# Optimization experiments

Hardware: AMD Instinct MI355X
Metric: run time of the kernel (lower is better)

Reference implementation:

```python
import jax, jax.numpy as jnp
import numpy as np

NUM_GRAPHS = 32   # point clouds per batch
PTS = 1024        # points per cloud (equal-size graphs; batch = node_idx // PTS)
NUM_FEAT = 14
DIM = 64
K = 30            # kNN includes the self-edge (distance 0), as torch_cluster.knn does


def _edge_conv(xb, W1, b1, W2, b2):
    # xb: [B, P, F] node features, per-graph dynamic kNN EdgeConv with max aggregation
    s = jnp.sum(xb * xb, axis=-1)                                   # [B, P]
    d = s[:, :, None] + s[:, None, :] - 2.0 * jnp.einsum('bpf,bqf->bpq', xb, xb)
    idx = jax.lax.top_k(-d, K)[1]                                   # [B, P, K]
    xj = jax.vmap(lambda xg, ig: xg[ig])(xb, idx)                   # [B, P, K, F]
    xi = xb[:, :, None, :]
    e = jnp.concatenate([jnp.broadcast_to(xi, xj.shape), xj - xi], axis=-1)  # [B,P,K,2F]
    h = jax.nn.relu(e @ W1 + b1)
    h = jax.nn.relu(h @ W2 + b2)
    return jnp.max(h, axis=2)                                       # [B, P, DIM]


def setup_inputs() -> dict:
    key = jax.random.key(0)
    ks = jax.random.split(key, 24)
    N = NUM_GRAPHS * PTS

    def w(i, shape):
        scale = shape[0] ** -0.5 if len(shape) > 1 else 0.02
        return jax.random.normal(ks[i], shape, jnp.float32) * scale

    return dict(
        x=jax.random.normal(ks[0], (N, NUM_FEAT), jnp.float32),
        batch=jnp.arange(N, dtype=jnp.int32) // PTS,
        c1w1=w(1, (2 * NUM_FEAT, DIM)), c1b1=w(2, (DIM,)), c1w2=w(3, (DIM, DIM)), c1b2=w(4, (DIM,)),
        c2w1=w(5, (2 * DIM, DIM)), c2b1=w(6, (DIM,)), c2w2=w(7, (DIM, DIM)), c2b2=w(8, (DIM,)),
        c3w1=w(9, (2 * DIM, DIM)), c3b1=w(10, (DIM,)), c3w2=w(11, (DIM, DIM)), c3b2=w(12, (DIM,)),
        lw=w(13, (3 * DIM, 1024)), lb=w(14, (1024,)),
        hw1=w(15, (1024, 256)), hb1=w(16, (256,)),
        hw2=w(17, (256, 128)), hb2=w(18, (128,)),
        hw3=w(19, (128, DIM)), hb3=w(20, (DIM,)),
    )


def reference(x, batch, c1w1, c1b1, c1w2, c1b2, c2w1, c2b1, c2w2, c2b2,
              c3w1, c3b1, c3w2, c3b2, lw, lb, hw1, hb1, hw2, hb2, hw3, hb3):
    # batch encodes equal-size graphs of PTS nodes -> reshape to [B, P, F]
    xb = x.reshape(NUM_GRAPHS, PTS, -1)
    x1 = _edge_conv(xb, c1w1, c1b1, c1w2, c1b2)
    x2 = _edge_conv(x1, c2w1, c2b1, c2w2, c2b2)
    x3 = _edge_conv(x2, c3w1, c3b1, c3w2, c3b2)
    h = jnp.concatenate([x1, x2, x3], axis=-1).reshape(-1, 3 * DIM)  # [N, 192]
    h = jax.nn.relu(h @ lw + lb)      # lin1: MLP([3*dim, 1024])
    h = jax.nn.relu(h @ hw1 + hb1)    # MLP([1024, 256]); dropout = identity at eval
    h = jax.nn.relu(h @ hw2 + hb2)    # MLP([256, 128]); dropout = identity at eval
    return h @ hw3 + hb3              # Lin(128, dim)
```

## Files before the change

kernel.cpp:

```cpp
#include <hip/hip_runtime.h>
#include <hip/hip_bf16.h>
#include <float.h>

#define NG    32
#define PTS   1024
#define NPTS  (NG*PTS)
#define KNN   30
#define DIM   64
#define CHUNK 8192

typedef __attribute__((ext_vector_type(8))) short bf16x8;
typedef __attribute__((ext_vector_type(4))) float f32x4;
typedef unsigned short ushort_t;

template<int F>
__global__ __launch_bounds__(256) void prep_k(const float* __restrict__ X, int ldx,
                                              float* __restrict__ S32,
                                              double* __restrict__ S64,
                                              float* __restrict__ XT) {
    int p = blockIdx.x * 256 + threadIdx.x;
    float s32 = 0.f;
    double s64 = 0.0;
    #pragma unroll
    for (int f = 0; f < F; ++f) {
        float v = X[(size_t)p * ldx + f];
        s32 = fmaf(v, v, s32);
        s64 = fma((double)v, (double)v, s64);
        XT[(size_t)f * NPTS + p] = v;
    }
    S32[p] = s32;
    S64[p] = s64;
}

__global__ __launch_bounds__(256) void smax_k(const float* __restrict__ S32,
                                              float* __restrict__ SMAX,
                                              int* __restrict__ ovf_cnt) {
    if (blockIdx.x == 0 && threadIdx.x == 0) *ovf_cnt = 0;
    int g = blockIdx.x;
    int lane = threadIdx.x & 63, wv = threadIdx.x >> 6;
    float m = 0.f;
    for (int t = threadIdx.x; t < PTS; t += 256) m = fmaxf(m, S32[(size_t)g * PTS + t]);
    #pragma unroll
    for (int off = 32; off; off >>= 1) m = fmaxf(m, __shfl_xor(m, off));
    __shared__ float wm[4];
    if (lane == 0) wm[wv] = m;
    __syncthreads();
    if (threadIdx.x == 0)
        SMAX[g] = fmaxf(fmaxf(wm[0], wm[1]), fmaxf(wm[2], wm[3]));
}

template<int F>
__global__ __launch_bounds__(256) void knn_k(const float* __restrict__ X, int ldx,
                                             const float* __restrict__ XT,
                                             const float* __restrict__ S32,
                                             const double* __restrict__ S64,
                                             const float* __restrict__ SMAX,
                                             int* __restrict__ IDX,
                                             int* __restrict__ ovf_cnt,
                                             int* __restrict__ ovf_list) {
    constexpr int FP = (F + 3) & ~3;
    int wv = threadIdx.x >> 6;
    int lane = threadIdx.x & 63;
    int i0 = blockIdx.x * 16;
    int base = i0 & ~(PTS - 1);
    __shared__ __align__(16) float xis[16][FP];
    __shared__ int surv[4][4][64];
    for (int l = threadIdx.x; l < 16 * F; l += 256) {
        int pt = l / F, f = l - pt * F;
        xis[pt][f] = X[(size_t)(i0 + pt) * ldx + f];
    }
    __syncthreads();

    float si[4];
    #pragma unroll
    for (int ii = 0; ii < 4; ++ii) si[ii] = S32[i0 + wv * 4 + ii];
    float smax = SMAX[i0 >> 10];

    float d32[4][16];
    #pragma unroll
    for (int ii = 0; ii < 4; ++ii)
        #pragma unroll
        for (int r = 0; r < 16; ++r) d32[ii][r] = 0.f;

    constexpr int F4 = F & ~3;
    for (int f4 = 0; f4 < F4; f4 += 4) {
        float4 xi[4];
        #pragma unroll
        for (int ii = 0; ii < 4; ++ii)
            xi[ii] = *reinterpret_cast<const float4*>(&xis[wv * 4 + ii][f4]);
        #pragma unroll
        for (int fo = 0; fo < 4; ++fo) {
            int f = f4 + fo;
            #pragma unroll
            for (int m = 0; m < 4; ++m) {
                const float4 xj = *reinterpret_cast<const float4*>(
                    &XT[(size_t)f * NPTS + base + (m << 8) + (lane << 2)]);
                #pragma unroll
                for (int ii = 0; ii < 4; ++ii) {
                    float xif = (fo == 0) ? xi[ii].x : (fo == 1) ? xi[ii].y
                               : (fo == 2) ? xi[ii].z : xi[ii].w;
                    d32[ii][m * 4 + 0] = fmaf(xif, xj.x, d32[ii][m * 4 + 0]);
                    d32[ii][m * 4 + 1] = fmaf(xif, xj.y, d32[ii][m * 4 + 1]);
                    d32[ii][m * 4 + 2] = fmaf(xif, xj.z, d32[ii][m * 4 + 2]);
                    d32[ii][m * 4 + 3] = fmaf(xif, xj.w, d32[ii][m * 4 + 3]);
                }
            }
        }
    }
    for (int f = F4; f < F; ++f) {
        float xif[4];
        #pragma unroll
        for (int ii = 0; ii < 4; ++ii) xif[ii] = xis[wv * 4 + ii][f];
        #pragma unroll
        for (int m = 0; m < 4; ++m) {
            const float4 xj = *reinterpret_cast<const float4*>(
                &XT[(size_t)f * NPTS + base + (m << 8) + (lane << 2)]);
            #pragma unroll
            for (int ii = 0; ii < 4; ++ii) {
                d32[ii][m * 4 + 0] = fmaf(xif[ii], xj.x, d32[ii][m * 4 + 0]);
                d32[ii][m * 4 + 1] = fmaf(xif[ii], xj.y, d32[ii][m * 4 + 1]);
                d32[ii][m * 4 + 2] = fmaf(xif[ii], xj.z, d32[ii][m * 4 + 2]);
                d32[ii][m * 4 + 3] = fmaf(xif[ii], xj.w, d32[ii][m * 4 + 3]);
            }
        }
    }
    #pragma unroll
    for (int m = 0; m < 4; ++m) {
        const float4 sj = *reinterpret_cast<const float4*>(&S32[base + (m << 8) + (lane << 2)]);
        #pragma unroll
        for (int ii = 0; ii < 4; ++ii) {
            d32[ii][m * 4 + 0] = (si[ii] + sj.x) - 2.f * d32[ii][m * 4 + 0];
            d32[ii][m * 4 + 1] = (si[ii] + sj.y) - 2.f * d32[ii][m * 4 + 1];
            d32[ii][m * 4 + 2] = (si[ii] + sj.z) - 2.f * d32[ii][m * 4 + 2];
            d32[ii][m * 4 + 3] = (si[ii] + sj.w) - 2.f * d32[ii][m * 4 + 3];
        }
    }

    const unsigned long long below = (1ull << lane) - 1;
    #pragma unroll
    for (int ii = 0; ii < 4; ++ii) {
        int i = i0 + wv * 4 + ii;
        float lo = -1.f, hi = 2.f * (si[ii] + smax) + 1.f;
        for (int it = 0; it < 32; ++it) {
            float piv = 0.5f * (lo + hi);
            int cnt = 0;
            #pragma unroll
            for (int r = 0; r < 16; ++r)
                cnt += __popcll(__ballot(d32[ii][r] <= piv));
            if (cnt >= KNN) { hi = piv; if (cnt <= 56) break; }
            else lo = piv;
        }
        float T = hi + 1.6e-5f * (si[ii] + smax);

        int total = 0;
        #pragma unroll
        for (int r = 0; r < 16; ++r) {
            bool pred = d32[ii][r] <= T;
            unsigned long long mask = __ballot(pred);
            if (pred) {
                int slot = total + __popcll(mask & below);
                if (slot < 64)
                    surv[wv][ii][slot] = ((r >> 2) << 8) + (lane << 2) + (r & 3);
            }
            total += __popcll(mask);
        }
        if (total > 64) {
            if (lane == 0) ovf_list[atomicAdd(ovf_cnt, 1)] = i;
            continue;
        }
        __builtin_amdgcn_wave_barrier();
        asm volatile("s_waitcnt lgkmcnt(0)" ::: "memory");

        double d64 = DBL_MAX;
        int jabs = 0x7fffffff;
        if (lane < total) {
            int jl = surv[wv][ii][lane];
            jabs = base + jl;
            const float* xj = X + (size_t)jabs * ldx;
            double dot = 0.0;
            #pragma unroll
            for (int f = 0; f < F; ++f)
                dot = fma((double)xis[wv * 4 + ii][f], (double)xj[f], dot);
            d64 = (S64[i] + S64[jabs]) - 2.0 * dot;
        }
        #pragma unroll
        for (int k = 2; k <= 64; k <<= 1) {
            #pragma unroll
            for (int s = k >> 1; s > 0; s >>= 1) {
                double od = __shfl_xor(d64, s);
                int oj = __shfl_xor(jabs, s);
                bool otherSmaller = (od < d64) || (od == d64 && oj < jabs);
                bool keepSmaller = (((lane & k) == 0) == ((lane & s) == 0));
                if (otherSmaller == keepSmaller) { d64 = od; jabs = oj; }
            }
        }
        if (lane < KNN) IDX[(size_t)i * KNN + lane] = jabs;
        __builtin_amdgcn_wave_barrier();
    }
}

template<int F>
__global__ __launch_bounds__(256) void fb_k(const float* __restrict__ X, int ldx,
                                            const float* __restrict__ XT,
                                            const double* __restrict__ S64,
                                            int* __restrict__ IDX,
                                            const int* __restrict__ ovf_cnt,
                                            const int* __restrict__ ovf_list) {
    int wv = threadIdx.x >> 6, lane = threadIdx.x & 63;
    int novf = *ovf_cnt;
    __shared__ double xis[4][F];
    for (int t = blockIdx.x * 4 + wv; t < novf; t += 64 * 4) {
        int i = ovf_list[t];
        int base = i & ~(PTS - 1);
        if (lane < F) xis[wv][lane] = (double)X[(size_t)i * ldx + lane];
        __builtin_amdgcn_wave_barrier();
        asm volatile("s_waitcnt lgkmcnt(0)" ::: "memory");
        double dd[16];
        #pragma unroll
        for (int m = 0; m < 4; ++m) {
            int j0 = (m << 8) + (lane << 2);
            double d0 = 0.0, d1 = 0.0, d2 = 0.0, d3 = 0.0;
            #pragma unroll
            for (int f = 0; f < F; ++f) {
                double xif = xis[wv][f];
                const float4 xj = *reinterpret_cast<const float4*>(&XT[(size_t)f * NPTS + base + j0]);
                d0 = fma(xif, (double)xj.x, d0);
                d1 = fma(xif, (double)xj.y, d1);
                d2 = fma(xif, (double)xj.z, d2);
                d3 = fma(xif, (double)xj.w, d3);
            }
            dd[m * 4 + 0] = (S64[i] + S64[base + j0 + 0]) - 2.0 * d0;
            dd[m * 4 + 1] = (S64[i] + S64[base + j0 + 1]) - 2.0 * d1;
            dd[m * 4 + 2] = (S64[i] + S64[base + j0 + 2]) - 2.0 * d2;
            dd[m * 4 + 3] = (S64[i] + S64[base + j0 + 3]) - 2.0 * d3;
        }
        for (int k = 0; k < KNN; ++k) {
            double bd = DBL_MAX;
            int bj = 0x7fffffff;
            #pragma unroll
            for (int r = 0; r < 16; ++r) {
                int j = ((r >> 2) << 8) + (lane << 2) + (r & 3);
                if (dd[r] < bd) { bd = dd[r]; bj = j; }
            }
            #pragma unroll
            for (int off = 32; off; off >>= 1) {
                double od = __shfl_xor(bd, off);
                int oj = __shfl_xor(bj, off);
                if (od < bd || (od == bd && oj < bj)) { bd = od; bj = oj; }
            }
            if (((bj >> 2) & 63) == lane) {
                int r = ((bj >> 8) << 2) | (bj & 3);
                #pragma unroll
                for (int rr = 0; rr < 16; ++rr) if (rr == r) dd[rr] = DBL_MAX;
            }
            if (lane == 0) IDX[(size_t)i * KNN + k] = base + bj;
        }
        __builtin_amdgcn_wave_barrier();
    }
}

template<int F>
__global__ __launch_bounds__(256) void mg_k(const float* __restrict__ X, int ldx,
                                            const float* __restrict__ W1,
                                            const float* __restrict__ B1,
                                            float* __restrict__ Mo, float* __restrict__ Go) {
    int tid = blockIdx.x * 256 + threadIdx.x;
    int pp = tid >> 6, c = tid & 63;
    float m = B1[c], g = 0.f;
    #pragma unroll
    for (int f = 0; f < F; ++f) {
        float xv = X[(size_t)pp * ldx + f];
        float wt = W1[f * DIM + c];
        float wb = W1[(F + f) * DIM + c];
        m = fmaf(xv, wt - wb, m);
        g = fmaf(xv, wb, g);
    }
    Mo[(size_t)pp * DIM + c] = m;
    Go[(size_t)pp * DIM + c] = g;
}

__global__ __launch_bounds__(256) void edge_k(const int* __restrict__ IDX,
                                              const float* __restrict__ G,
                                              const float* __restrict__ Mb,
                                              const float* __restrict__ W2,
                                              const float* __restrict__ B2,
                                              float* __restrict__ OUT, int ldo) {
    __shared__ ushort_t w2hi[64][72], w2lo[64][72];
    __shared__ ushort_t h1hi[4][32][72], h1lo[4][32][72];
    int wv = threadIdx.x >> 6, lane = threadIdx.x & 63;
    int i = blockIdx.x * 4 + wv;
    int col16 = lane & 15, grp = lane >> 4, grp8 = (lane >> 4) << 3;

    for (int l = threadIdx.x; l < 4096; l += 256) {
        int c = l & 63, k = l >> 6;
        float w = W2[k * 64 + c];
        __hip_bfloat16 bh = __float2bfloat16(w);
        __hip_bfloat16 bl = __float2bfloat16(w - __bfloat162float(bh));
        w2hi[c][k] = *reinterpret_cast<ushort_t*>(&bh);
        w2lo[c][k] = *reinterpret_cast<ushort_t*>(&bl);
    }
    __syncthreads();

    float mi = Mb[(size_t)i * DIM + lane];
    const int* idxrow = IDX + (size_t)i * KNN;
    int idxv = (lane < KNN) ? idxrow[lane] : 0;
    float g[KNN];
    #pragma unroll
    for (int nb = 0; nb < KNN; ++nb) {
        int j = __shfl(idxv, nb);
        g[nb] = G[(size_t)j * DIM + lane];
    }
    #pragma unroll
    for (int nb = 0; nb < KNN; ++nb) {
        float h = fmaxf(mi + g[nb], 0.f);
        __hip_bfloat16 bh = __float2bfloat16(h);
        __hip_bfloat16 bl = __float2bfloat16(h - __bfloat162float(bh));
        h1hi[wv][nb][lane] = *reinterpret_cast<ushort_t*>(&bh);
        h1lo[wv][nb][lane] = *reinterpret_cast<ushort_t*>(&bl);
    }
    h1hi[wv][30][lane] = 0; h1lo[wv][30][lane] = 0;
    h1hi[wv][31][lane] = 0; h1lo[wv][31][lane] = 0;
    __builtin_amdgcn_wave_barrier();
    asm volatile("s_waitcnt lgkmcnt(0)" ::: "memory");

    bf16x8 ahi[2][2], alo[2][2];
    #pragma unroll
    for (int m = 0; m < 2; ++m)
        #pragma unroll
        for (int ks = 0; ks < 2; ++ks) {
            ahi[m][ks] = *reinterpret_cast<const bf16x8*>(&h1hi[wv][m * 16 + col16][ks * 32 + grp8]);
            alo[m][ks] = *reinterpret_cast<const bf16x8*>(&h1lo[wv][m * 16 + col16][ks * 32 + grp8]);
        }

    float myout = 0.f;
    #pragma unroll
    for (int n = 0; n < 4; ++n) {
        bf16x8 bhi[2], blo[2];
        #pragma unroll
        for (int ks = 0; ks < 2; ++ks) {
            bhi[ks] = *reinterpret_cast<const bf16x8*>(&w2hi[n * 16 + col16][ks * 32 + grp8]);
            blo[ks] = *reinterpret_cast<const bf16x8*>(&w2lo[n * 16 + col16][ks * 32 + grp8]);
        }
        f32x4 acc0 = {0.f, 0.f, 0.f, 0.f}, acc1 = {0.f, 0.f, 0.f, 0.f};
        #pragma unroll
        for (int ks = 0; ks < 2; ++ks) {
            acc0 = __builtin_amdgcn_mfma_f32_16x16x32_bf16(ahi[0][ks], bhi[ks], acc0, 0, 0, 0);
            acc1 = __builtin_amdgcn_mfma_f32_16x16x32_bf16(ahi[1][ks], bhi[ks], acc1, 0, 0, 0);
            acc0 = __builtin_amdgcn_mfma_f32_16x16x32_bf16(ahi[0][ks], blo[ks], acc0, 0, 0, 0);
            acc1 = __builtin_amdgcn_mfma_f32_16x16x32_bf16(ahi[1][ks], blo[ks], acc1, 0, 0, 0);
            acc0 = __builtin_amdgcn_mfma_f32_16x16x32_bf16(alo[0][ks], bhi[ks], acc0, 0, 0, 0);
            acc1 = __builtin_amdgcn_mfma_f32_16x16x32_bf16(alo[1][ks], bhi[ks], acc1, 0, 0, 0);
        }
        float cm = fmaxf(fmaxf(acc0[0], acc0[1]), fmaxf(acc0[2], acc0[3]));
        cm = fmaxf(cm, fmaxf(acc1[0], acc1[1]));
        if (grp < 3) cm = fmaxf(cm, fmaxf(acc1[2], acc1[3]));
        cm = fmaxf(cm, __shfl_xor(cm, 16));
        cm = fmaxf(cm, __shfl_xor(cm, 32));
        if (grp == n) myout = cm;
    }
    OUT[(size_t)i * ldo + lane] = fmaxf(myout + B2[lane], 0.f);
}

template<int TM, int TN, int BK, bool RELU>
__global__ __launch_bounds__(256) void gemm_k(const float* __restrict__ A, int Kd,
                                              const float* __restrict__ W, int N,
                                              const float* __restrict__ Bias,
                                              float* __restrict__ C) {
    constexpr int MM = TM / 16, MN = TN / 16;
    __shared__ __align__(16) float As_t[BK][TM + 4];
    __shared__ __align__(16) float Ws[BK][TN];
    int bm = blockIdx.y * TM, bn = blockIdx.x * TN;
    int tid = threadIdx.x;
    int tr = tid >> 4, tc = tid & 15;
    float acc[MM][MN] = {};
    for (int k0 = 0; k0 < Kd; k0 += BK) {
        #pragma unroll
        for (int l = tid; l < TM * (BK / 4); l += 256) {
            int r = l / (BK / 4), q = l & (BK / 4 - 1);
            const float4 a4 = *reinterpret_cast<const float4*>(&A[(size_t)(bm + r) * Kd + k0 + 4 * q]);
            As_t[4 * q + 0][r] = a4.x;
            As_t[4 * q + 1][r] = a4.y;
            As_t[4 * q + 2][r] = a4.z;
            As_t[4 * q + 3][r] = a4.w;
        }
        #pragma unroll
        for (int l = tid; l < BK * (TN / 4); l += 256) {
            int r = l / (TN / 4), q = l & (TN / 4 - 1);
            *reinterpret_cast<float4*>(&Ws[r][4 * q]) =
                *reinterpret_cast<const float4*>(&W[(size_t)(k0 + r) * N + bn + 4 * q]);
        }
        __syncthreads();
        #pragma unroll
        for (int kk = 0; kk < BK; ++kk) {
            float a[MM], w[MN];
            #pragma unroll
            for (int u = 0; u < MM; u += 4) {
                const float4 v4 = *reinterpret_cast<const float4*>(&As_t[kk][tr * MM + u]);
                a[u] = v4.x; a[u + 1] = v4.y; a[u + 2] = v4.z; a[u + 3] = v4.w;
            }
            #pragma unroll
            for (int v = 0; v < MN; v += 4) {
                const float4 v4 = *reinterpret_cast<const float4*>(&Ws[kk][tc * MN + v]);
                w[v] = v4.x; w[v + 1] = v4.y; w[v + 2] = v4.z; w[v + 3] = v4.w;
            }
            #pragma unroll
            for (int u = 0; u < MM; ++u)
                #pragma unroll
                for (int v = 0; v < MN; ++v)
                    acc[u][v] = fmaf(a[u], w[v], acc[u][v]);
        }
        __syncthreads();
    }
    #pragma unroll
    for (int u = 0; u < MM; ++u) {
        int row = bm + tr * MM + u;
        #pragma unroll
        for (int v = 0; v < MN; v += 4) {
            int col = bn + tc * MN + v;
            float4 o;
            o.x = acc[u][v + 0] + Bias[col + 0];
            o.y = acc[u][v + 1] + Bias[col + 1];
            o.z = acc[u][v + 2] + Bias[col + 2];
            o.w = acc[u][v + 3] + Bias[col + 3];
            if (RELU) {
                o.x = fmaxf(o.x, 0.f); o.y = fmaxf(o.y, 0.f);
                o.z = fmaxf(o.z, 0.f); o.w = fmaxf(o.w, 0.f);
            }
            *reinterpret_cast<float4*>(&C[(size_t)row * N + col]) = o;
        }
    }
}

template<int F>
static void run_conv(const float* Xin, int ldx,
                     const float* W1, const float* B1,
                     const float* W2, const float* B2,
                     float* OUT, int ldo,
                     float* XT, float* S32, double* S64, float* SMAX,
                     float* Mb, float* Gb, int* IDX,
                     int* ovf_cnt, int* ovf_list,
                     hipStream_t stream) {
    prep_k<F><<<NPTS / 256, 256, 0, stream>>>(Xin, ldx, S32, S64, XT);
    smax_k<<<NG, 256, 0, stream>>>(S32, SMAX, ovf_cnt);
    knn_k<F><<<NPTS / 16, 256, 0, stream>>>(Xin, ldx, XT, S32, S64, SMAX, IDX,
                                            ovf_cnt, ovf_list);
    fb_k<F><<<64, 256, 0, stream>>>(Xin, ldx, XT, S64, IDX, ovf_cnt, ovf_list);
    mg_k<F><<<NPTS * DIM / 256, 256, 0, stream>>>(Xin, ldx, W1, B1, Mb, Gb);
    edge_k<<<NPTS / 4, 256, 0, stream>>>(IDX, Gb, Mb, W2, B2, OUT, ldo);
}

extern "C" void kernel_launch(void* const* d_in, const int* in_sizes, int n_in,
                              void* d_out, int out_size, void* d_ws, size_t ws_size,
                              hipStream_t stream) {
    (void)in_sizes; (void)n_in; (void)out_size; (void)ws_size;
    const float* x    = (const float*)d_in[0];
    const float* c1w1 = (const float*)d_in[2];  const float* c1b1 = (const float*)d_in[3];
    const float* c1w2 = (const float*)d_in[4];  const float* c1b2 = (const float*)d_in[5];
    const float* c2w1 = (const float*)d_in[6];  const float* c2b1 = (const float*)d_in[7];
    const float* c2w2 = (const float*)d_in[8];  const float* c2b2 = (const float*)d_in[9];
    const float* c3w1 = (const float*)d_in[10]; const float* c3b1 = (const float*)d_in[11];
    const float* c3w2 = (const float*)d_in[12]; const float* c3b2 = (const float*)d_in[13];
    const float* lw   = (const float*)d_in[14]; const float* lb   = (const float*)d_in[15];
    const float* hw1  = (const float*)d_in[16]; const float* hb1  = (const float*)d_in[17];
    const float* hw2  = (const float*)d_in[18]; const float* hb2  = (const float*)d_in[19];
    const float* hw3  = (const float*)d_in[20]; const float* hb3  = (const float*)d_in[21];
    float* out = (float*)d_out;

    float* XC  = (float*)d_ws;
    int*   IDX = (int*)(XC + (size_t)NPTS * 192);
    int*   ovf_cnt  = IDX + (size_t)NPTS * KNN;
    int*   ovf_list = ovf_cnt + 1;
    float* SCR = (float*)(ovf_list + NPTS + 1);
    float*  XT   = SCR;
    double* S64  = (double*)(XT + (size_t)64 * NPTS);
    float*  S32  = (float*)(S64 + NPTS);
    float*  SMAX = S32 + NPTS;
    float*  Mb   = SMAX + 64;
    float*  Gb   = Mb + (size_t)NPTS * DIM;
    float* H1 = SCR;
    float* H2 = H1 + (size_t)CHUNK * 1024;
    float* H3 = H2 + (size_t)CHUNK * 256;

    run_conv<14>(x,        14,  c1w1, c1b1, c1w2, c1b2, XC + 0,   192,
                 XT, S32, S64, SMAX, Mb, Gb, IDX, ovf_cnt, ovf_list, stream);
    run_conv<64>(XC + 0,   192, c2w1, c2b1, c2w2, c2b2, XC + 64,  192,
                 XT, S32, S64, SMAX, Mb, Gb, IDX, ovf_cnt, ovf_list, stream);
    run_conv<64>(XC + 64,  192, c3w1, c3b1, c3w2, c3b2, XC + 128, 192,
                 XT, S32, S64, SMAX, Mb, Gb, IDX, ovf_cnt, ovf_list, stream);

    for (int ch = 0; ch < 4; ++ch) {
        const float* a0 = XC + (size_t)ch * CHUNK * 192;
        float* o0 = out + (size_t)ch * CHUNK * 64;
        gemm_k<128, 128, 16, true ><<<dim3(1024 / 128, CHUNK / 128), 256, 0, stream>>>(a0, 192,  lw,  1024, lb,  H1);
        gemm_k< 64, 128, 16, true ><<<dim3(256  / 128, CHUNK / 64 ), 256, 0, stream>>>(H1, 1024, hw1, 256,  hb1, H2);
        gemm_k< 64, 128, 16, true ><<<dim3(128  / 128, CHUNK / 64 ), 256, 0, stream>>>(H2, 256,  hw2, 128,  hb2, H3);
        gemm_k< 64,  64, 16, false><<<dim3(64   / 64 , CHUNK / 64 ), 256, 0, stream>>>(H3, 128,  hw3, 64,   hb3, o0);
    }
}
```

Before: 1.616 ms.

## Move the two large head GEMMs to split-bf16 MFMA kernels

Replaces the fp32 SIMT GEMMs for lin1 (192->1024) and the first head layer (1024->256) with a new MFMA kernel that uses a three-term hi/lo bf16 split to stay close to fp32 accuracy. Weights are pre-split and transposed by a small conversion kernel. The 1024-wide intermediate is stored as bf16 hi/lo pairs instead of fp32, which keeps its memory traffic the same while removing reconversion. In exchange it costs extra conversion launches and a small loss of precision from dropping the lo*lo term.

Measured after the change: 1.397 ms. -13.6%, faster.

```diff
diff --git a/kernel.cpp b/kernel.cpp
--- a/kernel.cpp
+++ b/kernel.cpp
@@ -12,6 +12,14 @@
 typedef __attribute__((ext_vector_type(8))) short bf16x8;
 typedef __attribute__((ext_vector_type(4))) float f32x4;
 typedef unsigned short ushort_t;
+
+__device__ inline void bfsplit(float v, ushort_t& h, ushort_t& l) {
+    __hip_bfloat16 bh = __float2bfloat16(v);
+    float r = v - __bfloat162float(bh);
+    __hip_bfloat16 bl = __float2bfloat16(r);
+    h = *reinterpret_cast<ushort_t*>(&bh);
+    l = *reinterpret_cast<ushort_t*>(&bl);
+}
 
 template<int F>
 __global__ __launch_bounds__(256) void prep_k(const float* __restrict__ X, int ldx,
@@ -293,11 +301,7 @@
 
     for (int l = threadIdx.x; l < 4096; l += 256) {
         int c = l & 63, k = l >> 6;
-        float w = W2[k * 64 + c];
-        __hip_bfloat16 bh = __float2bfloat16(w);
-        __hip_bfloat16 bl = __float2bfloat16(w - __bfloat162float(bh));
-        w2hi[c][k] = *reinterpret_cast<ushort_t*>(&bh);
-        w2lo[c][k] = *reinterpret_cast<ushort_t*>(&bl);
+        bfsplit(W2[k * 64 + c], w2hi[c][k], w2lo[c][k]);
     }
     __syncthreads();
 
@@ -313,10 +317,7 @@
     #pragma unroll
     for (int nb = 0; nb < KNN; ++nb) {
         float h = fmaxf(mi + g[nb], 0.f);
-        __hip_bfloat16 bh = __float2bfloat16(h);
-        __hip_bfloat16 bl = __float2bfloat16(h - __bfloat162float(bh));
-        h1hi[wv][nb][lane] = *reinterpret_cast<ushort_t*>(&bh);
-        h1lo[wv][nb][lane] = *reinterpret_cast<ushort_t*>(&bl);
+        bfsplit(h, h1hi[wv][nb][lane], h1lo[wv][nb][lane]);
     }
     h1hi[wv][30][lane] = 0; h1lo[wv][30][lane] = 0;
     h1hi[wv][31][lane] = 0; h1lo[wv][31][lane] = 0;
@@ -359,6 +360,112 @@
         if (grp == n) myout = cm;
     }
     OUT[(size_t)i * ldo + lane] = fmaxf(myout + B2[lane], 0.f);
+}
+
+__global__ __launch_bounds__(256) void wcvt_k(const float* __restrict__ W, int K, int N,
+                                              ushort_t* __restrict__ Th,
+                                              ushort_t* __restrict__ Tl) {
+    int idx = blockIdx.x * 256 + threadIdx.x;
+    if (idx >= K * N) return;
+    int k = idx / N, n = idx - k * N;
+    ushort_t h, l;
+    bfsplit(W[idx], h, l);
+    Th[(size_t)n * K + k] = h;
+    Tl[(size_t)n * K + k] = l;
+}
+
+template<bool A32, bool OUT16, bool RELU>
+__global__ __launch_bounds__(256) void gemmx_k(
+    const float* __restrict__ Afp,
+    const ushort_t* __restrict__ Agh, const ushort_t* __restrict__ Agl, int Kd,
+    const ushort_t* __restrict__ Bth, const ushort_t* __restrict__ Btl,
+    int N, const float* __restrict__ Bias,
+    float* __restrict__ Cfp, ushort_t* __restrict__ Cgh, ushort_t* __restrict__ Cgl) {
+    constexpr int BM = 128, BN = 128, BKP = 40;
+    __shared__ ushort_t Ah[BM][BKP], Al[BM][BKP], Bh[BN][BKP], Bl[BN][BKP];
+    int tid = threadIdx.x;
+    int lane = tid & 63, wv = tid >> 6;
+    int wr = wv >> 1, wc = wv & 1;
+    int col16 = lane & 15, grp = lane >> 4, grp8 = grp << 3;
+    int bm = blockIdx.y * BM, bn = blockIdx.x * BN;
+    f32x4 acc[4][4];
+    #pragma unroll
+    for (int mf = 0; mf < 4; ++mf)
+        #pragma unroll
+        for (int nf = 0; nf < 4; ++nf) acc[mf][nf] = (f32x4){0.f, 0.f, 0.f, 0.f};
+
+    for (int k0 = 0; k0 < Kd; k0 += 32) {
+        if constexpr (A32) {
+            for (int l = tid; l < BM * 8; l += 256) {
+                int r = l >> 3, c4 = (l & 7) << 2;
+                const float4 a = *reinterpret_cast<const float4*>(&Afp[(size_t)(bm + r) * Kd + k0 + c4]);
+                ushort4 h4, l4;
+                bfsplit(a.x, h4.x, l4.x);
+                bfsplit(a.y, h4.y, l4.y);
+                bfsplit(a.z, h4.z, l4.z);
+                bfsplit(a.w, h4.w, l4.w);
+                *reinterpret_cast<ushort4*>(&Ah[r][c4]) = h4;
+                *reinterpret_cast<ushort4*>(&Al[r][c4]) = l4;
+            }
+        } else {
+            for (int l = tid; l < BM * 4; l += 256) {
+                int r = l >> 2, q = (l & 3) << 3;
+                *reinterpret_cast<uint4*>(&Ah[r][q]) =
+                    *reinterpret_cast<const uint4*>(&Agh[(size_t)(bm + r) * Kd + k0 + q]);
+                *reinterpret_cast<uint4*>(&Al[r][q]) =
+                    *reinterpret_cast<const uint4*>(&Agl[(size_t)(bm + r) * Kd + k0 + q]);
+            }
+        }
+        for (int l = tid; l < BN * 4; l += 256) {
+            int n = l >> 2, q = (l & 3) << 3;
+            *reinterpret_cast<uint4*>(&Bh[n][q]) =
+                *reinterpret_cast<const uint4*>(&Bth[(size_t)(bn + n) * Kd + k0 + q]);
+            *reinterpret_cast<uint4*>(&Bl[n][q]) =
+                *reinterpret_cast<const uint4*>(&Btl[(size_t)(bn + n) * Kd + k0 + q]);
+        }
+        __syncthreads();
+
+        bf16x8 afh[4], afl[4], bfh[4], bfl[4];
+        #pragma unroll
+        for (int mf = 0; mf < 4; ++mf) {
+            afh[mf] = *reinterpret_cast<const bf16x8*>(&Ah[wr * 64 + mf * 16 + col16][grp8]);
+            afl[mf] = *reinterpret_cast<const bf16x8*>(&Al[wr * 64 + mf * 16 + col16][grp8]);
+        }
+        #pragma unroll
+        for (int nf = 0; nf < 4; ++nf) {
+            bfh[nf] = *reinterpret_cast<const bf16x8*>(&Bh[wc * 64 + nf * 16 + col16][grp8]);
+            bfl[nf] = *reinterpret_cast<const bf16x8*>(&Bl[wc * 64 + nf * 16 + col16][grp8]);
+        }
+        #pragma unroll
+        for (int mf = 0; mf < 4; ++mf)
+            #pragma unroll
+            for (int nf = 0; nf < 4; ++nf) {
+                acc[mf][nf] = __builtin_amdgcn_mfma_f32_16x16x32_bf16(afh[mf], bfh[nf], acc[mf][nf], 0, 0, 0);
+                acc[mf][nf] = __builtin_amdgcn_mfma_f32_16x16x32_bf16(afh[mf], bfl[nf], acc[mf][nf], 0, 0, 0);
+                acc[mf][nf] = __builtin_amdgcn_mfma_f32_16x16x32_bf16(afl[mf], bfh[nf], acc[mf][nf], 0, 0, 0);
+            }
+        __syncthreads();
+    }
+
+    #pragma unroll
+    for (int nf = 0; nf < 4; ++nf) {
+        int col = bn + wc * 64 + nf * 16 + col16;
+        float b = Bias[col];
+        #pragma unroll
+        for (int mf = 0; mf < 4; ++mf) {
+            #pragma unroll
+            for (int rg = 0; rg < 4; ++rg) {
+                int row = bm + wr * 64 + mf * 16 + grp * 4 + rg;
+                float v = acc[mf][nf][rg] + b;
+                if (RELU) v = fmaxf(v, 0.f);
+                if constexpr (OUT16) {
+                    bfsplit(v, Cgh[(size_t)row * N + col], Cgl[(size_t)row * N + col]);
+                } else {
+                    Cfp[(size_t)row * N + col] = v;
+                }
+            }
+        }
+    }
 }
 
 template<int TM, int TN, int BK, bool RELU>
@@ -477,9 +584,14 @@
     float*  SMAX = S32 + NPTS;
     float*  Mb   = SMAX + 64;
     float*  Gb   = Mb + (size_t)NPTS * DIM;
-    float* H1 = SCR;
-    float* H2 = H1 + (size_t)CHUNK * 1024;
-    float* H3 = H2 + (size_t)CHUNK * 256;
+    ushort_t* H1h = (ushort_t*)SCR;
+    ushort_t* H1l = H1h + (size_t)CHUNK * 1024;
+    float* H2 = (float*)(H1l + (size_t)CHUNK * 1024);
+    float* H3 = (float*)H1h;
+    ushort_t* Wlwh = (ushort_t*)(H2 + (size_t)CHUNK * 256);
+    ushort_t* Wlwl = Wlwh + 192 * 1024;
+    ushort_t* Wh1h = Wlwl + 192 * 1024;
+    ushort_t* Wh1l = Wh1h + 1024 * 256;
 
     run_conv<14>(x,        14,  c1w1, c1b1, c1w2, c1b2, XC + 0,   192,
                  XT, S32, S64, SMAX, Mb, Gb, IDX, ovf_cnt, ovf_list, stream);
@@ -488,12 +600,17 @@
     run_conv<64>(XC + 64,  192, c3w1, c3b1, c3w2, c3b2, XC + 128, 192,
                  XT, S32, S64, SMAX, Mb, Gb, IDX, ovf_cnt, ovf_list, stream);
 
+    wcvt_k<<<(192 * 1024 + 255) / 256, 256, 0, stream>>>(lw,  192,  1024, Wlwh, Wlwl);
+    wcvt_k<<<(1024 * 256 + 255) / 256, 256, 0, stream>>>(hw1, 1024, 256,  Wh1h, Wh1l);
+
     for (int ch = 0; ch < 4; ++ch) {
         const float* a0 = XC + (size_t)ch * CHUNK * 192;
         float* o0 = out + (size_t)ch * CHUNK * 64;
-        gemm_k<128, 128, 16, true ><<<dim3(1024 / 128, CHUNK / 128), 256, 0, stream>>>(a0, 192,  lw,  1024, lb,  H1);
-        gemm_k< 64, 128, 16, true ><<<dim3(256  / 128, CHUNK / 64 ), 256, 0, stream>>>(H1, 1024, hw1, 256,  hb1, H2);
-        gemm_k< 64, 128, 16, true ><<<dim3(128  / 128, CHUNK / 64 ), 256, 0, stream>>>(H2, 256,  hw2, 128,  hb2, H3);
-        gemm_k< 64,  64, 16, false><<<dim3(64   / 64 , CHUNK / 64 ), 256, 0, stream>>>(H3, 128,  hw3, 64,   hb3, o0);
-    }
-}
+        gemmx_k<true, true, true><<<dim3(1024 / 128, CHUNK / 128), 256, 0, stream>>>(
+            a0, nullptr, nullptr, 192, Wlwh, Wlwl, 1024, lb, nullptr, H1h, H1l);
+        gemmx_k<false, false, true><<<dim3(256 / 128, CHUNK / 128), 256, 0, stream>>>(
+            nullptr, H1h, H1l, 1024, Wh1h, Wh1l, 256, hb1, H2, nullptr, nullptr);
+        gemm_k<64, 128, 16, true ><<<dim3(128 / 128, CHUNK / 64), 256, 0, stream>>>(H2, 256, hw2, 128, hb2, H3);
+        gemm_k<64, 64, 16, false><<<dim3(64 / 64,   CHUNK / 64), 256, 0, stream>>>(H3, 128, hw3, 64,  hb3, o0);
+    }
+}
```
